# Kernel tuning notes

Measured on AMD Instinct MI355X. Metric: run time of the kernel, lower is better.

Reference implementation:

```python
import jax, jax.numpy as jnp
import numpy as np

N_NODES, N_EDGES, B = 100000, 200000, 2048
ND, ED, HID, OUT, HEADS = 64, 16, 512, 512, 4

# dummy-graph topology: central node 0 -> features 1..6, plus self loops (GATv2 default)
D_SRC = jnp.array([0, 0, 0, 0, 0, 0, 0, 1, 2, 3, 4, 5, 6])
D_DST = jnp.array([1, 2, 3, 4, 5, 6, 0, 1, 2, 3, 4, 5, 6])


def setup_inputs() -> dict:
    key = jax.random.key(0)
    ks = jax.random.split(key, 40)
    p = lambda k, sh: (jax.random.normal(k, sh, dtype=jnp.float32) * 0.05)
    inp = {
        'x': jax.random.normal(ks[0], (N_NODES, ND), dtype=jnp.float32),
        'edge_index': jax.random.randint(ks[1], (2, N_EDGES), 0, N_NODES),
        'edge_attr': jax.random.normal(ks[2], (N_EDGES, ED), dtype=jnp.float32),
        'batch': jnp.sort(jax.random.randint(ks[3], (N_NODES,), 0, B)),
        'ecfp': jax.random.uniform(ks[4], (B, OUT), dtype=jnp.float32),
        'topo': jax.random.uniform(ks[5], (B, OUT), dtype=jnp.float32),
        'maccs': jax.random.uniform(ks[6], (B, OUT), dtype=jnp.float32),
        'estate': jax.random.uniform(ks[7], (B, OUT), dtype=jnp.float32),
        'rdkit2d': jax.random.normal(ks[8], (B, OUT), dtype=jnp.float32),
        'phar2d': jax.random.normal(ks[9], (B, OUT), dtype=jnp.float32),
        # GINEConv 1: nn = Linear(ND, HID); edge proj Linear(ED, ND)
        'g1_W': p(ks[10], (ND, HID)), 'g1_b': p(ks[11], (HID,)),
        'e1_W': p(ks[12], (ED, ND)), 'e1_b': p(ks[13], (ND,)),
        'bn1_g': jnp.ones((HID,), jnp.float32), 'bn1_b': jnp.zeros((HID,), jnp.float32),
        # GINEConv 2: nn = Linear(HID, OUT); edge proj Linear(ED, HID)
        'g2_W': p(ks[14], (HID, OUT)), 'g2_b': p(ks[15], (OUT,)),
        'e2_W': p(ks[16], (ED, HID)), 'e2_b': p(ks[17], (HID,)),
        'bn2_g': jnp.ones((OUT,), jnp.float32), 'bn2_b': jnp.zeros((OUT,), jnp.float32),
        # GATv2Conv 1: OUT -> HID, heads, concat=False
        'gat1_Wl': p(ks[18], (OUT, HEADS * HID)), 'gat1_bl': p(ks[19], (HEADS * HID,)),
        'gat1_Wr': p(ks[20], (OUT, HEADS * HID)), 'gat1_br': p(ks[21], (HEADS * HID,)),
        'gat1_att': p(ks[22], (HEADS, HID)), 'gat1_bias': p(ks[23], (HID,)),
        'bn3_g': jnp.ones((HID,), jnp.float32), 'bn3_b': jnp.zeros((HID,), jnp.float32),
        # GATv2Conv 2: HID -> HID
        'gat2_Wl': p(ks[24], (HID, HEADS * HID)), 'gat2_bl': p(ks[25], (HEADS * HID,)),
        'gat2_Wr': p(ks[26], (HID, HEADS * HID)), 'gat2_br': p(ks[27], (HEADS * HID,)),
        'gat2_att': p(ks[28], (HEADS, HID)), 'gat2_bias': p(ks[29], (HID,)),
        'bn4_g': jnp.ones((HID,), jnp.float32), 'bn4_b': jnp.zeros((HID,), jnp.float32),
        'fc_W': p(ks[30], (HID, 1)), 'fc_b': p(ks[31], (1,)),
    }
    return inp


def _bn_eval(h, g, b):
    # PyG BatchNorm in eval mode with fresh running stats (mean=0, var=1)
    return g * (h * (1.0 / np.sqrt(1.0 + 1e-5))) + b


def _gatv2(z, Wl, bl, Wr, br, att, bias):
    # z: [B, 7, Cin]; GATv2Conv with self-loops, concat=False (mean over heads)
    Bn, Nn, _ = z.shape
    Hh, Co = att.shape
    gl = (z @ Wl + bl).reshape(Bn, Nn, Hh, Co)  # source transform
    gr = (z @ Wr + br).reshape(Bn, Nn, Hh, Co)  # target transform
    e = jax.nn.leaky_relu(gl[:, D_SRC] + gr[:, D_DST], 0.2)  # [B, 13, H, Co]
    logits = jnp.einsum('behc,hc->beh', e, att)  # [B, 13, H]

    def seg_softmax(lg):
        m = jax.ops.segment_max(lg, D_DST, num_segments=7)
        ex = jnp.exp(lg - m[D_DST])
        s = jax.ops.segment_sum(ex, D_DST, num_segments=7)
        return ex / s[D_DST]

    alpha = jax.vmap(seg_softmax)(logits)  # [B, 13, H]
    msg = gl[:, D_SRC] * alpha[..., None]  # [B, 13, H, Co]
    out = jax.vmap(lambda mm: jax.ops.segment_sum(mm, D_DST, num_segments=7))(msg)
    return out.mean(axis=2) + bias  # [B, 7, Co]


def reference(x, edge_index, edge_attr, batch, ecfp, topo, maccs, estate, rdkit2d, phar2d,
              g1_W, g1_b, e1_W, e1_b, bn1_g, bn1_b,
              g2_W, g2_b, e2_W, e2_b, bn2_g, bn2_b,
              gat1_Wl, gat1_bl, gat1_Wr, gat1_br, gat1_att, gat1_bias, bn3_g, bn3_b,
              gat2_Wl, gat2_bl, gat2_Wr, gat2_br, gat2_att, gat2_bias, bn4_g, bn4_b,
              fc_W, fc_b):
    N = x.shape[0]
    Bg = ecfp.shape[0]
    src, dst = edge_index[0], edge_index[1]
    # GINEConv 1: msg = relu(x_j + W_e e), sum-aggr, out = Lin(x + aggr) (eps=0)
    m = jax.nn.relu(x[src] + (edge_attr @ e1_W + e1_b))
    h = (x + jax.ops.segment_sum(m, dst, num_segments=N)) @ g1_W + g1_b
    h = jax.nn.relu(_bn_eval(h, bn1_g, bn1_b))  # dropout = identity (eval)
    # GINEConv 2
    m2 = jax.nn.relu(h[src] + (edge_attr @ e2_W + e2_b))
    h2 = (h + jax.ops.segment_sum(m2, dst, num_segments=N)) @ g2_W + g2_b
    h2 = jax.nn.relu(_bn_eval(h2, bn2_g, bn2_b))
    # global mean pool
    sums = jax.ops.segment_sum(h2, batch, num_segments=Bg)
    cnts = jax.ops.segment_sum(jnp.ones((N,), h2.dtype), batch, num_segments=Bg)
    graph_out = sums / jnp.maximum(cnts, 1.0)[:, None]  # [B, OUT]
    # batched 7-node dummy graphs (node 0 = graph embedding, 1..6 = features)
    xn = jnp.stack([graph_out, ecfp, topo, maccs, estate, rdkit2d, phar2d], axis=1)
    z = _gatv2(xn, gat1_Wl, gat1_bl, gat1_Wr, gat1_br, gat1_att, gat1_bias)
    z = jax.nn.relu(_bn_eval(z, bn3_g, bn3_b))
    z = _gatv2(z, gat2_Wl, gat2_bl, gat2_Wr, gat2_br, gat2_att, gat2_bias)
    z = jax.nn.relu(_bn_eval(z, bn4_g, bn4_b))
    return z[:, 0, :] @ fc_W + fc_b  # [B, 1]
```

## Files before the change

### kernel.cpp

```cpp
#include <hip/hip_runtime.h>
#include <hip/hip_bf16.h>

#define N_NODESC 100000
#define N_EDGESC 200000
#define BG 2048
#define NDIM 64
#define EDIM 16

typedef __bf16 bf16x8 __attribute__((ext_vector_type(8)));
typedef float f32x4 __attribute__((ext_vector_type(4)));

static __device__ __forceinline__ float bn_inv() { return 0.9999950000374997f; }

__device__ __forceinline__ void gl2lds16(const void* g, void* l) {
    __builtin_amdgcn_global_load_lds(
        (const __attribute__((address_space(1))) unsigned int*)g,
        (__attribute__((address_space(3))) unsigned int*)l, 16, 0, 0);
}

__global__ void zero_f4(float4* __restrict__ p, int n4) {
    int i = blockIdx.x * 256 + threadIdx.x;
    if (i < n4) p[i] = make_float4(0.f, 0.f, 0.f, 0.f);
}
__global__ void zero_int(int* __restrict__ p, int n) {
    int i = blockIdx.x * 256 + threadIdx.x;
    if (i < n) p[i] = 0;
}
__global__ void zero_out(float* __restrict__ p, int n) {
    int i = blockIdx.x * 256 + threadIdx.x;
    if (i < n) p[i] = 0.f;
}

__global__ void hist_dst(const int* __restrict__ dst, int* __restrict__ deg) {
    int i = blockIdx.x * 256 + threadIdx.x;
    if (i < N_EDGESC) atomicAdd(&deg[dst[i]], 1);
}
__global__ void scan_bsums(const int* __restrict__ deg, int* __restrict__ bsum, int n) {
    __shared__ int ls[256];
    int b = blockIdx.x, t = threadIdx.x;
    int s = 0;
#pragma unroll
    for (int j = 0; j < 4; j++) {
        int i = b * 1024 + t * 4 + j;
        if (i < n) s += deg[i];
    }
    ls[t] = s;
    __syncthreads();
    for (int off = 128; off; off >>= 1) {
        if (t < off) ls[t] += ls[t + off];
        __syncthreads();
    }
    if (t == 0) bsum[b] = ls[0];
}
__global__ void scan_top(int* __restrict__ bsum, int nb, int* __restrict__ total) {
    if (threadIdx.x == 0) {
        int acc = 0;
        for (int i = 0; i < nb; i++) { int v = bsum[i]; bsum[i] = acc; acc += v; }
        *total = acc;
    }
}
__global__ void scan_final(const int* __restrict__ deg, const int* __restrict__ bsum,
                           int* __restrict__ rowptr, int* __restrict__ cursor, int n) {
    __shared__ int ls[256];
    int b = blockIdx.x, t = threadIdx.x;
    int v[4], s = 0;
#pragma unroll
    for (int j = 0; j < 4; j++) {
        int i = b * 1024 + t * 4 + j;
        v[j] = (i < n) ? deg[i] : 0;
        s += v[j];
    }
    ls[t] = s;
    __syncthreads();
    int run = s;
    for (int off = 1; off < 256; off <<= 1) {
        int add = (t >= off) ? ls[t - off] : 0;
        __syncthreads();
        ls[t] += add;
        __syncthreads();
    }
    int excl = ls[t] - run + bsum[b];
#pragma unroll
    for (int j = 0; j < 4; j++) {
        int i = b * 1024 + t * 4 + j;
        if (i < n) { rowptr[i] = excl; cursor[i] = excl; excl += v[j]; }
    }
}
__global__ void scatter_eid(const int* __restrict__ dst, int* __restrict__ cursor,
                            int* __restrict__ eid) {
    int e = blockIdx.x * 256 + threadIdx.x;
    if (e < N_EDGESC) {
        int p = atomicAdd(&cursor[dst[e]], 1);
        eid[p] = e;
    }
}

__global__ void transpose_w(const float* __restrict__ W, __hip_bfloat16* __restrict__ hi,
                            int K, int N) {
    __shared__ float t[64][65];
    int k0 = blockIdx.x * 64, n0 = blockIdx.y * 64;
    int tid = threadIdx.x, tx = tid & 63, ty = tid >> 6;
    for (int r = ty; r < 64; r += 4) t[r][tx] = W[(size_t)(k0 + r) * N + n0 + tx];
    __syncthreads();
    for (int r = ty; r < 64; r += 4)
        hi[(size_t)(n0 + r) * K + k0 + tx] = __float2bfloat16(t[tx][r]);
}

__global__ void concat_bias(const float* __restrict__ a, const float* __restrict__ b,
                            float* __restrict__ o) {
    int i = blockIdx.x * 256 + threadIdx.x;
    if (i < 2048) { o[i] = a[i]; o[2048 + i] = b[i]; }
}

#define G1_NPW 8
__global__ __launch_bounds__(256, 2) void gine1_gather(
    const float* __restrict__ x, const int* __restrict__ srcv, const float* __restrict__ ea,
    const float* __restrict__ e1W, const float* __restrict__ e1b,
    const int* __restrict__ rowptr, const int* __restrict__ eid,
    __hip_bfloat16* __restrict__ xin) {
    int tid = threadIdx.x;
    int wave = tid >> 6, lane = tid & 63;
    float wreg[16];
#pragma unroll
    for (int k = 0; k < 16; k++) wreg[k] = e1W[k * 64 + lane];
    float bb = e1b[lane];
    int nbase = (blockIdx.x * 4 + wave) * G1_NPW;
#pragma unroll 1
    for (int it = 0; it < G1_NPW; it++) {
        int n = nbase + it;
        if (n >= N_NODESC) return;
        float acc = x[(size_t)n * 64 + lane];
        int beg = rowptr[n], end = rowptr[n + 1];
        for (int idx = beg; idx < end; idx++) {
            int e = eid[idx], s = srcv[e];
            const float4* ef = (const float4*)(ea + (size_t)e * 16);
            float4 e0 = ef[0], e1 = ef[1], e2 = ef[2], e3 = ef[3];
            float p = bb;
            p = fmaf(e0.x, wreg[0], p);  p = fmaf(e0.y, wreg[1], p);
            p = fmaf(e0.z, wreg[2], p);  p = fmaf(e0.w, wreg[3], p);
            p = fmaf(e1.x, wreg[4], p);  p = fmaf(e1.y, wreg[5], p);
            p = fmaf(e1.z, wreg[6], p);  p = fmaf(e1.w, wreg[7], p);
            p = fmaf(e2.x, wreg[8], p);  p = fmaf(e2.y, wreg[9], p);
            p = fmaf(e2.z, wreg[10], p); p = fmaf(e2.w, wreg[11], p);
            p = fmaf(e3.x, wreg[12], p); p = fmaf(e3.y, wreg[13], p);
            p = fmaf(e3.z, wreg[14], p); p = fmaf(e3.w, wreg[15], p);
            acc += fmaxf(x[(size_t)s * 64 + lane] + p, 0.f);
        }
        xin[(size_t)n * 64 + lane] = __float2bfloat16(acc);
    }
}

#define G2_NPB 16
__global__ __launch_bounds__(256, 2) void gine2_gather(
    const __hip_bfloat16* __restrict__ h, const int* __restrict__ srcv,
    const float* __restrict__ ea, const float* __restrict__ e2W,
    const float* __restrict__ e2b, const int* __restrict__ rowptr,
    const int* __restrict__ eid, __hip_bfloat16* __restrict__ a2, int n0, int n1) {
    int tid = threadIdx.x;
    int half = tid >> 7, lt = tid & 127;
    float wreg[4][16], breg[4];
#pragma unroll
    for (int j = 0; j < 4; j++) {
        int c = lt * 4 + j;
        breg[j] = e2b[c];
#pragma unroll
        for (int k = 0; k < 16; k++) wreg[j][k] = e2W[k * 512 + c];
    }
    int nbase = n0 + blockIdx.x * G2_NPB + half;
#pragma unroll 1
    for (int it = 0; it < G2_NPB / 2; it++) {
        int n = nbase + it * 2;
        if (n >= n1) return;
        short4 hv = *(const short4*)((const short*)(h + (size_t)n * 512) + lt * 4);
        const __hip_bfloat16* hb = (const __hip_bfloat16*)&hv;
        float acc[4];
#pragma unroll
        for (int j = 0; j < 4; j++) acc[j] = __bfloat162float(hb[j]);
        int beg = rowptr[n], end = rowptr[n + 1];
        for (int idx = beg; idx < end; idx++) {
            int e = eid[idx], s = srcv[e];
            const float4* ef = (const float4*)(ea + (size_t)e * 16);
            float4 e0 = ef[0], e1 = ef[1], e2v = ef[2], e3 = ef[3];
            short4 sv = *(const short4*)((const short*)(h + (size_t)s * 512) + lt * 4);
            const __hip_bfloat16* sb = (const __hip_bfloat16*)&sv;
#pragma unroll
            for (int j = 0; j < 4; j++) {
                float p = breg[j];
                p = fmaf(e0.x, wreg[j][0], p);  p = fmaf(e0.y, wreg[j][1], p);
                p = fmaf(e0.z, wreg[j][2], p);  p = fmaf(e0.w, wreg[j][3], p);
                p = fmaf(e1.x, wreg[j][4], p);  p = fmaf(e1.y, wreg[j][5], p);
                p = fmaf(e1.z, wreg[j][6], p);  p = fmaf(e1.w, wreg[j][7], p);
                p = fmaf(e2v.x, wreg[j][8], p); p = fmaf(e2v.y, wreg[j][9], p);
                p = fmaf(e2v.z, wreg[j][10], p);p = fmaf(e2v.w, wreg[j][11], p);
                p = fmaf(e3.x, wreg[j][12], p); p = fmaf(e3.y, wreg[j][13], p);
                p = fmaf(e3.z, wreg[j][14], p); p = fmaf(e3.w, wreg[j][15], p);
                acc[j] += fmaxf(__bfloat162float(sb[j]) + p, 0.f);
            }
        }
        __hip_bfloat16 o[4];
#pragma unroll
        for (int j = 0; j < 4; j++) o[j] = __float2bfloat16(acc[j]);
        *(short4*)((short*)(a2 + (size_t)(n - n0) * 512) + lt * 4) = *(const short4*)o;
    }
}

template <int MODE>
__global__ __launch_bounds__(256, 4) void mfma_gemm(
    const __hip_bfloat16* __restrict__ A, const __hip_bfloat16* __restrict__ Bhi,
    int M, int K, int N, const float* __restrict__ bias, const float* __restrict__ bng,
    const float* __restrict__ bnb, const int* __restrict__ batch,
    float* __restrict__ psum, __hip_bfloat16* __restrict__ Cout) {
    __shared__ short As[128 * 32];
    __shared__ short Bh[128 * 32];
    int r0 = blockIdx.y * 128;
    int n0 = blockIdx.x * 128;
    int tid = threadIdx.x;
    int lane = tid & 63;
    int wv = tid >> 6;
    int wm = (wv >> 1) * 64, wn = (wv & 1) * 64;

    f32x4 acc[4][4];
#pragma unroll
    for (int i = 0; i < 4; i++)
#pragma unroll
        for (int j = 0; j < 4; j++) acc[i][j] = (f32x4){0.f, 0.f, 0.f, 0.f};

    int rowA0 = tid >> 2, cbA0 = tid & 3;
    int rowA1 = (tid + 256) >> 2, cbA1 = tid & 3;
    for (int k0 = 0; k0 < K; k0 += 32) {
        __syncthreads();
        {
            int g0 = r0 + rowA0; if (g0 >= M) g0 = M - 1;
            int g1 = r0 + rowA1; if (g1 >= M) g1 = M - 1;
            gl2lds16(A + (size_t)g0 * K + k0 + cbA0 * 8, As + wv * 512);
            gl2lds16(A + (size_t)g1 * K + k0 + cbA1 * 8, As + 2048 + wv * 512);
            gl2lds16(Bhi + (size_t)(n0 + rowA0) * K + k0 + cbA0 * 8, Bh + wv * 512);
            gl2lds16(Bhi + (size_t)(n0 + rowA1) * K + k0 + cbA1 * 8, Bh + 2048 + wv * 512);
        }
        __syncthreads();
        int fi = lane & 15, kb = (lane >> 4) * 8;
        bf16x8 af[4], bhf[4];
#pragma unroll
        for (int mi = 0; mi < 4; mi++)
            af[mi] = *(const bf16x8*)(As + (wm + mi * 16 + fi) * 32 + kb);
#pragma unroll
        for (int ni = 0; ni < 4; ni++)
            bhf[ni] = *(const bf16x8*)(Bh + (wn + ni * 16 + fi) * 32 + kb);
#pragma unroll
        for (int mi = 0; mi < 4; mi++)
#pragma unroll
            for (int ni = 0; ni < 4; ni++)
                acc[mi][ni] = __builtin_amdgcn_mfma_f32_16x16x32_bf16(af[mi], bhf[ni],
                                                                     acc[mi][ni], 0, 0, 0);
    }
    int col_l = lane & 15, quad = lane >> 4;
#pragma unroll
    for (int mi = 0; mi < 4; mi++) {
        int rbase = r0 + wm + mi * 16 + quad * 4;
#pragma unroll
        for (int ni = 0; ni < 4; ni++) {
            int gcol = n0 + wn + ni * 16 + col_l;
            if (MODE == 0) {
                float b0 = bias[gcol];
#pragma unroll
                for (int reg = 0; reg < 4; reg++) {
                    int grow = rbase + reg;
                    if (grow < M)
                        Cout[(size_t)grow * N + gcol] = __float2bfloat16(acc[mi][ni][reg] + b0);
                }
            } else {
                float b0 = bias[gcol], g0 = bng[gcol], bb0 = bnb[gcol];
                float vv[4];
#pragma unroll
                for (int reg = 0; reg < 4; reg++)
                    vv[reg] = fmaxf(fmaf((acc[mi][ni][reg] + b0) * bn_inv(), g0, bb0), 0.f);
                if (MODE == 1) {
#pragma unroll
                    for (int reg = 0; reg < 4; reg++) {
                        int grow = rbase + reg;
                        if (grow < M) Cout[(size_t)grow * 512 + gcol] = __float2bfloat16(vv[reg]);
                    }
                } else {
                    if (rbase + 3 < M && batch[rbase] == batch[rbase + 3]) {
                        atomicAdd(&psum[(size_t)batch[rbase] * 512 + gcol],
                                  (vv[0] + vv[1]) + (vv[2] + vv[3]));
                    } else {
#pragma unroll
                        for (int reg = 0; reg < 4; reg++) {
                            int grow = rbase + reg;
                            if (grow < M)
                                atomicAdd(&psum[(size_t)batch[grow] * 512 + gcol], vv[reg]);
                        }
                    }
                }
            }
        }
    }
}

__global__ void count_nodes(const int* __restrict__ batch, float* __restrict__ cnt) {
    int i = blockIdx.x * 256 + threadIdx.x;
    if (i < N_NODESC) atomicAdd(&cnt[batch[i]], 1.0f);
}

__global__ void build_xn(const float* __restrict__ psum, const float* __restrict__ cnt,
                         const float* __restrict__ ecfp, const float* __restrict__ topo,
                         const float* __restrict__ maccs, const float* __restrict__ estate,
                         const float* __restrict__ rdkit2d, const float* __restrict__ phar2d,
                         __hip_bfloat16* __restrict__ xn) {
    int i = blockIdx.x * 256 + threadIdx.x;
    if (i >= BG * 512) return;
    int bidx = i >> 9, c = i & 511;
    float cv = fmaxf(cnt[bidx], 1.0f);
    __hip_bfloat16* o = xn + (size_t)bidx * 7 * 512;
    o[c] = __float2bfloat16(psum[i] / cv);
    o[512 + c] = __float2bfloat16(ecfp[i]);
    o[2 * 512 + c] = __float2bfloat16(topo[i]);
    o[3 * 512 + c] = __float2bfloat16(maccs[i]);
    o[4 * 512 + c] = __float2bfloat16(estate[i]);
    o[5 * 512 + c] = __float2bfloat16(rdkit2d[i]);
    o[6 * 512 + c] = __float2bfloat16(phar2d[i]);
}

__global__ void gat_attn(const __hip_bfloat16* __restrict__ cg,
                         const float* __restrict__ att, const float* __restrict__ bias,
                         const float* __restrict__ bng, const float* __restrict__ bnb,
                         __hip_bfloat16* __restrict__ zout) {
    int b = blockIdx.x;
    int tid = threadIdx.x;
    int wave = tid >> 6, lane = tid & 63;
    __shared__ float logits[13][4];
    __shared__ float alpha[13][4];
    const size_t base = (size_t)b * 7 * 4096;
    for (int p = wave; p < 52; p += 4) {
        int e = p >> 2, hh = p & 3;
        int se = (e < 7) ? 0 : (e - 6);
        int de = (e < 6) ? (e + 1) : ((e == 6) ? 0 : (e - 6));
        const __hip_bfloat16* glp = cg + base + (size_t)se * 4096 + hh * 512;
        const __hip_bfloat16* grp = cg + base + (size_t)de * 4096 + 2048 + hh * 512;
        const float* ap = att + hh * 512;
        float s = 0.f;
#pragma unroll
        for (int j = 0; j < 8; j++) {
            int c = lane + j * 64;
            float v = __bfloat162float(glp[c]) + __bfloat162float(grp[c]);
            v = (v >= 0.f) ? v : 0.2f * v;
            s = fmaf(v, ap[c], s);
        }
#pragma unroll
        for (int off = 32; off; off >>= 1) s += __shfl_down(s, off);
        if (lane == 0) logits[e][hh] = s;
    }
    __syncthreads();
    if (tid < 24) {
        int n = 1 + (tid >> 2), hh = tid & 3;
        float la = logits[n - 1][hh], lb = logits[6 + n][hh];
        float m = fmaxf(la, lb);
        float ea = __expf(la - m), eb = __expf(lb - m);
        float inv = 1.f / (ea + eb);
        alpha[n - 1][hh] = ea * inv;
        alpha[6 + n][hh] = eb * inv;
    } else if (tid < 28) {
        alpha[6][tid & 3] = 1.f;
    }
    __syncthreads();
    for (int i = tid; i < 7 * 512; i += 256) {
        int n = i >> 9, c = i & 511;
        float v = 0.f;
        if (n == 0) {
#pragma unroll
            for (int hh = 0; hh < 4; hh++)
                v = fmaf(alpha[6][hh],
                         __bfloat162float(cg[base + (size_t)hh * 512 + c]), v);
        } else {
#pragma unroll
            for (int hh = 0; hh < 4; hh++) {
                v = fmaf(alpha[n - 1][hh],
                         __bfloat162float(cg[base + (size_t)hh * 512 + c]), v);
                v = fmaf(alpha[6 + n][hh],
                         __bfloat162float(cg[base + (size_t)n * 4096 + hh * 512 + c]), v);
            }
        }
        v = fmaf(v, 0.25f, bias[c]);
        v = fmaf(v * bn_inv(), bng[c], bnb[c]);
        zout[(size_t)b * 7 * 512 + i] = __float2bfloat16(fmaxf(v, 0.f));
    }
}

__global__ void final_fc(const __hip_bfloat16* __restrict__ z, const float* __restrict__ fcW,
                         const float* __restrict__ fcb, float* __restrict__ out) {
    int b = blockIdx.x * 4 + (threadIdx.x >> 6);
    int lane = threadIdx.x & 63;
    if (b >= BG) return;
    const __hip_bfloat16* row = z + (size_t)b * 7 * 512;
    float s = 0.f;
#pragma unroll
    for (int j = 0; j < 8; j++)
        s = fmaf(__bfloat162float(row[lane + j * 64]), fcW[lane + j * 64], s);
#pragma unroll
    for (int off = 32; off; off >>= 1) s += __shfl_down(s, off);
    if (lane == 0) out[b] = s + fcb[0];
}

extern "C" void kernel_launch(void* const* d_in, const int* in_sizes, int n_in,
                              void* d_out, int out_size, void* d_ws, size_t ws_size,
                              hipStream_t stream) {
    const float* x = (const float*)d_in[0];
    const int* eidx = (const int*)d_in[1];
    const float* eattr = (const float*)d_in[2];
    const int* batch = (const int*)d_in[3];
    const float* ecfp = (const float*)d_in[4];
    const float* topo = (const float*)d_in[5];
    const float* maccs = (const float*)d_in[6];
    const float* estate = (const float*)d_in[7];
    const float* rdkit2d = (const float*)d_in[8];
    const float* phar2d = (const float*)d_in[9];
    const float* g1_W = (const float*)d_in[10];
    const float* g1_b = (const float*)d_in[11];
    const float* e1_W = (const float*)d_in[12];
    const float* e1_b = (const float*)d_in[13];
    const float* bn1_g = (const float*)d_in[14];
    const float* bn1_b = (const float*)d_in[15];
    const float* g2_W = (const float*)d_in[16];
    const float* g2_b = (const float*)d_in[17];
    const float* e2_W = (const float*)d_in[18];
    const float* e2_b = (const float*)d_in[19];
    const float* bn2_g = (const float*)d_in[20];
    const float* bn2_b = (const float*)d_in[21];
    const float* gat1_Wl = (const float*)d_in[22];
    const float* gat1_bl = (const float*)d_in[23];
    const float* gat1_Wr = (const float*)d_in[24];
    const float* gat1_br = (const float*)d_in[25];
    const float* gat1_att = (const float*)d_in[26];
    const float* gat1_bias = (const float*)d_in[27];
    const float* bn3_g = (const float*)d_in[28];
    const float* bn3_b = (const float*)d_in[29];
    const float* gat2_Wl = (const float*)d_in[30];
    const float* gat2_bl = (const float*)d_in[31];
    const float* gat2_Wr = (const float*)d_in[32];
    const float* gat2_br = (const float*)d_in[33];
    const float* gat2_att = (const float*)d_in[34];
    const float* gat2_bias = (const float*)d_in[35];
    const float* bn4_g = (const float*)d_in[36];
    const float* bn4_b = (const float*)d_in[37];
    const float* fc_W = (const float*)d_in[38];
    const float* fc_b = (const float*)d_in[39];
    float* out = (float*)d_out;

    const size_t NEEDED = 194682880ull;
    if (ws_size < NEEDED) {
        zero_out<<<(BG + 255) / 256, 256, 0, stream>>>(out, BG);
        return;
    }
    char* w = (char*)d_ws;
    __hip_bfloat16* H = (__hip_bfloat16*)w;
    __hip_bfloat16* CG = (__hip_bfloat16*)w;
    __hip_bfloat16* A2 = (__hip_bfloat16*)(w + 102400000);
    __hip_bfloat16* GW12 = (__hip_bfloat16*)(w + 117440512);
    __hip_bfloat16* GW34 = (__hip_bfloat16*)(w + 121634816);
    __hip_bfloat16* Z1B = (__hip_bfloat16*)(w + 125829120);
    float* B12 = (float*)(w + 140509184);
    float* B34 = (float*)(w + 140525568);

    char* C = w + 161120256;
    __hip_bfloat16* XIN = (__hip_bfloat16*)C;
    __hip_bfloat16* XNB = (__hip_bfloat16*)C;
    __hip_bfloat16* Z2B = (__hip_bfloat16*)(C + 14680064);
    int* ROWPTR = (int*)(C + 14680064);
    int* CURSOR = (int*)(C + 15080192);
    int* EID = (int*)(C + 15480320);
    int* DEG = (int*)(C + 16280320);
    __hip_bfloat16* G1W = (__hip_bfloat16*)(C + 16680320);
    __hip_bfloat16* G2W = (__hip_bfloat16*)(C + 16745856);
    int* BSUM = (int*)(C + 17270144);

    float* PS = (float*)(w + 190480384);
    float* PC = (float*)(w + 194674688);

    const int* src = eidx;
    const int* dst = eidx + N_EDGESC;

    zero_int<<<(N_NODESC + 255) / 256, 256, 0, stream>>>(DEG, N_NODESC);
    zero_f4<<<(BG * 512 / 4 + 255) / 256, 256, 0, stream>>>((float4*)PS, BG * 512 / 4);
    zero_f4<<<(BG / 4 + 255) / 256, 256, 0, stream>>>((float4*)PC, BG / 4);
    hist_dst<<<(N_EDGESC + 255) / 256, 256, 0, stream>>>(dst, DEG);
    const int NB = (N_NODESC + 1023) / 1024;
    scan_bsums<<<NB, 256, 0, stream>>>(DEG, BSUM, N_NODESC);
    scan_top<<<1, 64, 0, stream>>>(BSUM, NB, ROWPTR + N_NODESC);
    scan_final<<<NB, 256, 0, stream>>>(DEG, BSUM, ROWPTR, CURSOR, N_NODESC);
    scatter_eid<<<(N_EDGESC + 255) / 256, 256, 0, stream>>>(dst, CURSOR, EID);

    transpose_w<<<dim3(1, 8), 256, 0, stream>>>(g1_W, G1W, 64, 512);
    transpose_w<<<dim3(8, 8), 256, 0, stream>>>(g2_W, G2W, 512, 512);

    gine1_gather<<<(N_NODESC + 4 * G1_NPW - 1) / (4 * G1_NPW), 256, 0, stream>>>(
        x, src, eattr, e1_W, e1_b, ROWPTR, EID, XIN);
    mfma_gemm<1><<<dim3(4, (N_NODESC + 127) / 128), 256, 0, stream>>>(
        XIN, G1W, N_NODESC, 64, 512, g1_b, bn1_g, bn1_b, nullptr, nullptr, H);
    count_nodes<<<(N_NODESC + 255) / 256, 256, 0, stream>>>(batch, PC);

    for (int c0n = 0; c0n < N_NODESC; c0n += 50000) {
        int c1n = c0n + 50000;
        int rows = 50000;
        gine2_gather<<<(rows + G2_NPB - 1) / G2_NPB, 256, 0, stream>>>(
            H, src, eattr, e2_W, e2_b, ROWPTR, EID, A2, c0n, c1n);
        mfma_gemm<2><<<dim3(4, (rows + 127) / 128), 256, 0, stream>>>(
            A2, G2W, rows, 512, 512, g2_b, bn2_g, bn2_b, batch + c0n, PS, nullptr);
    }

    transpose_w<<<dim3(8, 32), 256, 0, stream>>>(gat1_Wl, GW12, 512, 2048);
    transpose_w<<<dim3(8, 32), 256, 0, stream>>>(gat1_Wr, GW12 + (size_t)2048 * 512, 512, 2048);
    transpose_w<<<dim3(8, 32), 256, 0, stream>>>(gat2_Wl, GW34, 512, 2048);
    transpose_w<<<dim3(8, 32), 256, 0, stream>>>(gat2_Wr, GW34 + (size_t)2048 * 512, 512, 2048);
    concat_bias<<<8, 256, 0, stream>>>(gat1_bl, gat1_br, B12);
    concat_bias<<<8, 256, 0, stream>>>(gat2_bl, gat2_br, B34);

    build_xn<<<(BG * 512) / 256, 256, 0, stream>>>(PS, PC, ecfp, topo, maccs, estate,
                                                   rdkit2d, phar2d, XNB);
    const int MGAT = BG * 7;
    dim3 ggrid(4096 / 128, MGAT / 128);
    mfma_gemm<0><<<ggrid, 256, 0, stream>>>(XNB, GW12, MGAT, 512, 4096, B12,
                                            nullptr, nullptr, nullptr, nullptr, CG);
    gat_attn<<<BG, 256, 0, stream>>>(CG, gat1_att, gat1_bias, bn3_g, bn3_b, Z1B);
    mfma_gemm<0><<<ggrid, 256, 0, stream>>>(Z1B, GW34, MGAT, 512, 4096, B34,
                                            nullptr, nullptr, nullptr, nullptr, CG);
    gat_attn<<<BG, 256, 0, stream>>>(CG, gat2_att, gat2_bias, bn4_g, bn4_b, Z2B);
    final_fc<<<BG / 4, 256, 0, stream>>>(Z2B, fc_W, fc_b, out);
}
```

Baseline: 1.053 ms.

## Double-buffer LDS tiles in MFMA GEMM to overlap loads with compute

The GEMM main loop now uses two LDS buffers for A and B tiles, issuing global-to-LDS loads for the next K-slice while MFMAs consume the current one, with one barrier per slice instead of two. Load addresses are also precomputed outside the loop, and launch bounds are raised to 5 blocks per SM. The aim is to hide global memory latency and cut barrier overhead, at the cost of doubled LDS use per block (32KB), which may limit occupancy, and tighter register pressure.

```diff
diff --git a/kernel.cpp b/kernel.cpp
--- a/kernel.cpp
+++ b/kernel.cpp
@@ -205,13 +205,15 @@
 }
 
 template <int MODE>
-__global__ __launch_bounds__(256, 4) void mfma_gemm(
+__global__ __launch_bounds__(256, 5) void mfma_gemm(
     const __hip_bfloat16* __restrict__ A, const __hip_bfloat16* __restrict__ Bhi,
     int M, int K, int N, const float* __restrict__ bias, const float* __restrict__ bng,
     const float* __restrict__ bnb, const int* __restrict__ batch,
     float* __restrict__ psum, __hip_bfloat16* __restrict__ Cout) {
-    __shared__ short As[128 * 32];
-    __shared__ short Bh[128 * 32];
+    __shared__ short As0[128 * 32];
+    __shared__ short Bh0[128 * 32];
+    __shared__ short As1[128 * 32];
+    __shared__ short Bh1[128 * 32];
     int r0 = blockIdx.y * 128;
     int n0 = blockIdx.x * 128;
     int tid = threadIdx.x;
@@ -226,33 +228,52 @@
         for (int j = 0; j < 4; j++) acc[i][j] = (f32x4){0.f, 0.f, 0.f, 0.f};
 
     int rowA0 = tid >> 2, cbA0 = tid & 3;
-    int rowA1 = (tid + 256) >> 2, cbA1 = tid & 3;
-    for (int k0 = 0; k0 < K; k0 += 32) {
-        __syncthreads();
-        {
-            int g0 = r0 + rowA0; if (g0 >= M) g0 = M - 1;
-            int g1 = r0 + rowA1; if (g1 >= M) g1 = M - 1;
-            gl2lds16(A + (size_t)g0 * K + k0 + cbA0 * 8, As + wv * 512);
-            gl2lds16(A + (size_t)g1 * K + k0 + cbA1 * 8, As + 2048 + wv * 512);
-            gl2lds16(Bhi + (size_t)(n0 + rowA0) * K + k0 + cbA0 * 8, Bh + wv * 512);
-            gl2lds16(Bhi + (size_t)(n0 + rowA1) * K + k0 + cbA1 * 8, Bh + 2048 + wv * 512);
-        }
-        __syncthreads();
+    int rowA1 = (tid + 256) >> 2;
+    int gA0 = r0 + rowA0; if (gA0 >= M) gA0 = M - 1;
+    int gA1 = r0 + rowA1; if (gA1 >= M) gA1 = M - 1;
+    const __hip_bfloat16* pA0 = A + (size_t)gA0 * K + cbA0 * 8;
+    const __hip_bfloat16* pA1 = A + (size_t)gA1 * K + cbA0 * 8;
+    const __hip_bfloat16* pB0 = Bhi + (size_t)(n0 + rowA0) * K + cbA0 * 8;
+    const __hip_bfloat16* pB1 = Bhi + (size_t)(n0 + rowA1) * K + cbA0 * 8;
+
+    auto stage = [&](short* Asb, short* Bhb, int koff) {
+        gl2lds16(pA0 + koff, Asb + wv * 512);
+        gl2lds16(pA1 + koff, Asb + 2048 + wv * 512);
+        gl2lds16(pB0 + koff, Bhb + wv * 512);
+        gl2lds16(pB1 + koff, Bhb + 2048 + wv * 512);
+    };
+    auto compute = [&](const short* Asb, const short* Bhb) {
         int fi = lane & 15, kb = (lane >> 4) * 8;
         bf16x8 af[4], bhf[4];
 #pragma unroll
         for (int mi = 0; mi < 4; mi++)
-            af[mi] = *(const bf16x8*)(As + (wm + mi * 16 + fi) * 32 + kb);
+            af[mi] = *(const bf16x8*)(Asb + (wm + mi * 16 + fi) * 32 + kb);
 #pragma unroll
         for (int ni = 0; ni < 4; ni++)
-            bhf[ni] = *(const bf16x8*)(Bh + (wn + ni * 16 + fi) * 32 + kb);
+            bhf[ni] = *(const bf16x8*)(Bhb + (wn + ni * 16 + fi) * 32 + kb);
 #pragma unroll
         for (int mi = 0; mi < 4; mi++)
 #pragma unroll
             for (int ni = 0; ni < 4; ni++)
                 acc[mi][ni] = __builtin_amdgcn_mfma_f32_16x16x32_bf16(af[mi], bhf[ni],
                                                                      acc[mi][ni], 0, 0, 0);
-    }
+    };
+
+    const int NT = K >> 5;
+    stage(As0, Bh0, 0);
+    __syncthreads();
+#pragma unroll 1
+    for (int t = 0; t < NT; t += 2) {
+        if (t + 1 < NT) stage(As1, Bh1, (t + 1) << 5);
+        compute(As0, Bh0);
+        __syncthreads();
+        if (t + 1 < NT) {
+            if (t + 2 < NT) stage(As0, Bh0, (t + 2) << 5);
+            compute(As1, Bh1);
+            __syncthreads();
+        }
+    }
+
     int col_l = lane & 15, quad = lane >> 4;
 #pragma unroll
     for (int mi = 0; mi < 4; mi++) {
```

Result: slower. 1.283 ms (+21.9%).
